# Kernel optimization log

Hardware: AMD Instinct MI355X
Metric: run time of the kernel (lower is better)

## Reference

```python
import jax, jax.numpy as jnp
import numpy as np

B, N = 4, 2048
EMB, HID = 64, 256
LENGTHSCALES = (0.5, 1.0, 2.0, 4.0)
H = len(LENGTHSCALES)
HEAD = HID // H  # 64, divides evenly
LAYERS = 4
IN_DIM = 3 + EMB + 3
EPS_LN = 1e-5


def _layer_norm(x, g, b):
    mu = jnp.mean(x, axis=-1, keepdims=True)
    var = jnp.mean((x - mu) ** 2, axis=-1, keepdims=True)
    return (x - mu) * jax.lax.rsqrt(var + EPS_LN) * g + b


def setup_inputs() -> dict:
    key = jax.random.key(0)
    ks = iter(jax.random.split(key, 32))
    p = lambda shape, s=0.02: jax.random.normal(next(ks), shape, jnp.float32) * s
    inp = {
        "latent_vars": jax.random.normal(next(ks), (B, N, 3), jnp.float32),
        "x_coords": jax.random.normal(next(ks), (B, N, 3), jnp.float32),
        "atom_embeddings": jax.random.normal(next(ks), (B, N, EMB), jnp.float32),
        # input MLP
        "in_W": p((IN_DIM, HID)), "in_b": jnp.zeros((HID,), jnp.float32),
        # per-layer kernel attention: per-head value projections + output projection
        "val_W": p((LAYERS, H, HID, HEAD)), "val_b": jnp.zeros((LAYERS, H, HEAD), jnp.float32),
        "attn_W": p((LAYERS, H * HEAD, HID)), "attn_b": jnp.zeros((LAYERS, HID), jnp.float32),
        # layer norms
        "ln1_g": jnp.ones((LAYERS, HID), jnp.float32), "ln1_b": jnp.zeros((LAYERS, HID), jnp.float32),
        "ln2_g": jnp.ones((LAYERS, HID), jnp.float32), "ln2_b": jnp.zeros((LAYERS, HID), jnp.float32),
        # FFN (hidden -> 2*hidden -> hidden)
        "ffn_W1": p((LAYERS, HID, 2 * HID)), "ffn_b1": jnp.zeros((LAYERS, 2 * HID), jnp.float32),
        "ffn_W2": p((LAYERS, 2 * HID, HID)), "ffn_b2": jnp.zeros((LAYERS, HID), jnp.float32),
        # output MLP
        "out_W1": p((HID, HID)), "out_b1": jnp.zeros((HID,), jnp.float32),
        "out_W2": p((HID, 3)), "out_b2": jnp.zeros((3,), jnp.float32),
    }
    return inp


def _forward(latent_vars, x_coords, atom_embeddings, in_W, in_b, val_W, val_b,
             attn_W, attn_b, ln1_g, ln1_b, ln2_g, ln2_b,
             ffn_W1, ffn_b1, ffn_W2, ffn_b2, out_W1, out_b1, out_W2, out_b2):
    # input MLP
    x = jnp.concatenate([x_coords, atom_embeddings, latent_vars], axis=-1)  # [B,N,70]
    feats = jax.nn.relu(x @ in_W + in_b)  # [B,N,HID]

    # RBF attention weights depend only on coords + fixed lengthscales -> compute once
    diff = x_coords[:, :, None, :] - x_coords[:, None, :, :]  # [B,N,N,3]
    d2 = jnp.sum(diff * diff, axis=-1)  # [B,N,N]
    ls2 = jnp.asarray(LENGTHSCALES, jnp.float32) ** 2  # [H]
    A = jnp.exp(-d2[None, :, :, :] / ls2[:, None, None, None])  # [H,B,N,N]
    A = A / (jnp.sum(A, axis=-1, keepdims=True) + 1e-8)

    for l in range(LAYERS):
        V = jnp.einsum('bnf,hfd->bnhd', feats, val_W[l]) + val_b[l]  # [B,N,H,HEAD]
        att = jnp.einsum('hbij,bjhd->bihd', A, V)  # [B,N,H,HEAD]
        att = att.reshape(att.shape[0], att.shape[1], H * HEAD) @ attn_W[l] + attn_b[l]
        feats = _layer_norm(feats + att, ln1_g[l], ln1_b[l])
        h = jax.nn.relu(feats @ ffn_W1[l] + ffn_b1[l]) @ ffn_W2[l] + ffn_b2[l]
        feats = _layer_norm(feats + h, ln2_g[l], ln2_b[l])

    return jax.nn.relu(feats @ out_W1 + out_b1) @ out_W2 + out_b2  # [B,N,3]


def reference(latent_vars, x_coords, atom_embeddings, in_W, in_b, val_W, val_b,
              attn_W, attn_b, ln1_g, ln1_b, ln2_g, ln2_b,
              ffn_W1, ffn_b1, ffn_W2, ffn_b2, out_W1, out_b1, out_W2, out_b2):
    return _forward(latent_vars, x_coords, atom_embeddings, in_W, in_b, val_W, val_b,
                    attn_W, attn_b, ln1_g, ln1_b, ln2_g, ln2_b,
                    ffn_W1, ffn_b1, ffn_W2, ffn_b2, out_W1, out_b1, out_W2, out_b2)
```

## Files before the change

### kernel.cpp

```cpp
#include <hip/hip_runtime.h>

#define B_ 4
#define N_ 2048
#define R_ (B_ * N_)
#define HID_ 256
#define EMB_ 64
#define IN_DIM_ 70
#define H_ 4
#define HEAD_ 64
#define FFN_ 512
#define LAYERS_ 4

typedef __attribute__((ext_vector_type(8))) short short8;
typedef __attribute__((ext_vector_type(4))) float f32x4;
typedef unsigned short ushort;

static __device__ __forceinline__ ushort f2bf(float f) {
    unsigned u = __builtin_bit_cast(unsigned, f);
    u += 0x7fffu + ((u >> 16) & 1u);
    return (ushort)(u >> 16);
}
static __device__ __forceinline__ float bf2f(ushort u) {
    unsigned x = ((unsigned)u) << 16;
    return __builtin_bit_cast(float, x);
}

#define GLOAD_LDS16(g, l)                                              \
    __builtin_amdgcn_global_load_lds(                                  \
        (const __attribute__((address_space(1))) void*)(g),            \
        (__attribute__((address_space(3))) void*)(l), 16, 0, 0)

#define MFMA16(a, b, c) __builtin_amdgcn_mfma_f32_16x16x32_bf16(a, b, c, 0, 0, 0)

__global__ __launch_bounds__(256) void pack_weights(const float* __restrict__ valW,
                                                    const float* __restrict__ attnW,
                                                    const float* __restrict__ ffnW1,
                                                    const float* __restrict__ ffnW2,
                                                    const float* __restrict__ outW1,
                                                    ushort* __restrict__ wp) {
    int idx = blockIdx.x * 256 + threadIdx.x;
    float v;
    if (idx < 262144) {
        int l = idx >> 16, c = (idx >> 8) & 255, k = idx & 255;
        v = valW[((l * 4 + (c >> 6)) * 256 + k) * 64 + (c & 63)];
    } else if (idx < 524288) {
        int i2 = idx - 262144;
        int l = i2 >> 16, c = (i2 >> 8) & 255, k = i2 & 255;
        v = attnW[l * 65536 + k * 256 + c];
    } else if (idx < 1048576) {
        int i2 = idx - 524288;
        int l = i2 >> 17, c = (i2 >> 8) & 511, k = i2 & 255;
        v = ffnW1[l * 131072 + k * 512 + c];
    } else if (idx < 1572864) {
        int i2 = idx - 1048576;
        int l = i2 >> 17, c = (i2 >> 9) & 255, k = i2 & 511;
        v = ffnW2[l * 131072 + k * 256 + c];
    } else {
        int i2 = idx - 1572864;
        int c = i2 >> 8, k = i2 & 255;
        v = outW1[k * 256 + c];
    }
    wp[idx] = f2bf(v);
}

__global__ __launch_bounds__(256) void input_mlp(const float* __restrict__ xc,
                                                 const float* __restrict__ emb,
                                                 const float* __restrict__ lat,
                                                 const float* __restrict__ W,
                                                 const float* __restrict__ b,
                                                 float* __restrict__ feats,
                                                 ushort* __restrict__ featsb) {
    __shared__ float xr[8][IN_DIM_ + 2];
    int t = threadIdx.x;
    int row0 = blockIdx.x * 8;
    for (int idx = t; idx < 8 * IN_DIM_; idx += 256) {
        int r = idx / IN_DIM_, f = idx % IN_DIM_;
        int rr = row0 + r;
        float v;
        if (f < 3)       v = xc[rr * 3 + f];
        else if (f < 67) v = emb[rr * EMB_ + (f - 3)];
        else             v = lat[rr * 3 + (f - 67)];
        xr[r][f] = v;
    }
    __syncthreads();
    float acc[8] = {0.f, 0.f, 0.f, 0.f, 0.f, 0.f, 0.f, 0.f};
    for (int f = 0; f < IN_DIM_; ++f) {
        float w = W[f * HID_ + t];
#pragma unroll
        for (int r = 0; r < 8; ++r) acc[r] += xr[r][f] * w;
    }
    float bb = b[t];
#pragma unroll
    for (int r = 0; r < 8; ++r) {
        float v = fmaxf(acc[r] + bb, 0.f);
        feats[(row0 + r) * HID_ + t] = v;
        featsb[(row0 + r) * HID_ + t] = f2bf(v);
    }
}

__global__ __launch_bounds__(256) void ebuild(const float* __restrict__ xc,
                                              ushort* __restrict__ E) {
    __shared__ float4 civ[64];
    __shared__ float4 cjv[512];
    int t = threadIdx.x;
    int jb = blockIdx.x;
    int ibl = blockIdx.y;
    int b = blockIdx.z;
    const float* xb = xc + (size_t)b * N_ * 3;
    if (t < 64) {
        const float* p = &xb[(ibl * 64 + t) * 3];
        float x = p[0], y = p[1], z = p[2];
        civ[t] = make_float4(x, y, z, x * x + y * y + z * z);
    }
#pragma unroll
    for (int s = 0; s < 2; ++s) {
        int j = s * 256 + t;
        const float* p = &xb[(jb * 512 + j) * 3];
        float x = p[0], y = p[1], z = p[2];
        cjv[j] = make_float4(x, y, z, x * x + y * y + z * z);
    }
    __syncthreads();
    int lane = t & 63, ig = t >> 6;
    float4 cj[8];
#pragma unroll
    for (int e = 0; e < 8; ++e) cj[e] = cjv[lane * 8 + e];
    const float ch0 = -4.f * 1.44269504088896f;
    ushort* Ebase = E + ((size_t)b * 2048 + ibl * 64) * 2048 + (size_t)jb * 512 + lane * 8;

    for (int r = 0; r < 16; ++r) {
        int i = ig * 16 + r;
        float4 ci = civ[i];
        float d[8];
#pragma unroll
        for (int e = 0; e < 8; ++e)
            d[e] = (ci.w + cj[e].w) -
                   2.f * (ci.x * cj[e].x + ci.y * cj[e].y + ci.z * cj[e].z);
        float ch = ch0;
#pragma unroll
        for (int h = 0; h < 4; ++h) {
            float ex[8];
#pragma unroll
            for (int e = 0; e < 8; ++e) ex[e] = exp2f(d[e] * ch);
            union { unsigned u[4]; uint4 v; } pk;
#pragma unroll
            for (int q = 0; q < 4; ++q)
                asm("v_cvt_pk_bf16_f32 %0, %1, %2"
                    : "=v"(pk.u[q]) : "v"(ex[2 * q]), "v"(ex[2 * q + 1]));
            *(uint4*)(Ebase + (size_t)h * 4 * 2048 * 2048 + (size_t)i * 2048) = pk.v;
            ch *= 0.25f;
        }
    }
}

__global__ __launch_bounds__(256, 2) void pv_gemm(const ushort* __restrict__ E,
                                                  const ushort* __restrict__ Vt,
                                                  ushort* __restrict__ attb) {
    __shared__ __align__(16) char lds[65536];
    int t = threadIdx.x;
    int l = t & 63, w = t >> 6;
    int lr = l & 15, g = l >> 4;

    int f = blockIdx.x;
    int xcd = f & 7, s = f >> 3;
    int combo = xcd * 2 + (s >> 5);
    int ib = s & 31;
    int b = combo & 3, h = combo >> 2;
    int i_base = ib * 64;
    int hc = h * 64;

    const ushort* Eb = E + (size_t)(h * 4 + b) * 2048 * 2048;
    int slot = t & 7, trow = t >> 3;

    const ushort* srcA[2];
    const ushort* srcB[2];
#pragma unroll
    for (int q = 0; q < 2; ++q) {
        int arw = q * 32 + trow;
        srcA[q] = Eb + (size_t)(i_base + arw) * 2048 + ((slot ^ (arw & 7)) << 3);
        srcB[q] = Vt + (size_t)(b * 256 + hc + arw) * 2048 + ((slot ^ (arw & 7)) << 3);
    }
    auto STAGE = [&](int c) {
        int buf = c & 3;
#pragma unroll
        for (int q = 0; q < 2; ++q)
            GLOAD_LDS16(srcA[q] + c * 64, lds + buf * 16384 + q * 4096 + t * 16);
#pragma unroll
        for (int q = 0; q < 2; ++q)
            GLOAD_LDS16(srcB[q] + c * 64, lds + buf * 16384 + 8192 + q * 4096 + t * 16);
    };

    f32x4 acc[4] = {};
    f32x4 accd = {};
    short8 ones = {0x3F80, 0x3F80, 0x3F80, 0x3F80, 0x3F80, 0x3F80, 0x3F80, 0x3F80};

    int arow = w * 16 + lr;
    int aoff = arow * 128;
    int sw_a = (arow & 7) << 4;

    auto COMPUTE = [&](int c) {
        const char* As = lds + (c & 3) * 16384;
        const char* Bs = As + 8192;
        short8 a0 = *(const short8*)(As + aoff + ((g * 16) ^ sw_a));
        short8 a1 = *(const short8*)(As + aoff + ((64 + g * 16) ^ sw_a));
        accd = MFMA16(a0, ones, accd);
        accd = MFMA16(a1, ones, accd);
#pragma unroll
        for (int n = 0; n < 4; ++n) {
            int cc = n * 16 + lr;
            const char* cb = Bs + cc * 128;
            int sw = (cc & 7) << 4;
            short8 b0 = *(const short8*)(cb + ((g * 16) ^ sw));
            short8 b1 = *(const short8*)(cb + ((64 + g * 16) ^ sw));
            acc[n] = MFMA16(a0, b0, acc[n]);
            acc[n] = MFMA16(a1, b1, acc[n]);
        }
    };

    STAGE(0);
    STAGE(1);
    STAGE(2);

    for (int c = 0; c < 30; ++c) {
        asm volatile("s_waitcnt vmcnt(8)" ::: "memory");
        __builtin_amdgcn_s_barrier();
        __builtin_amdgcn_sched_barrier(0);
        if (c < 29) STAGE(c + 3);
        COMPUTE(c);
    }
    asm volatile("s_waitcnt vmcnt(4)" ::: "memory");
    __builtin_amdgcn_s_barrier();
    __builtin_amdgcn_sched_barrier(0);
    COMPUTE(30);
    asm volatile("s_waitcnt vmcnt(0)" ::: "memory");
    __builtin_amdgcn_s_barrier();
    __builtin_amdgcn_sched_barrier(0);
    COMPUTE(31);

#pragma unroll
    for (int r = 0; r < 4; ++r) {
        float invd = 1.f / (accd[r] + 1e-8f);
        int row = i_base + w * 16 + g * 4 + r;
        size_t rb = ((size_t)b * N_ + row) * 256 + hc + lr;
#pragma unroll
        for (int n = 0; n < 4; ++n)
            attb[rb + n * 16] = f2bf(acc[n][r] * invd);
    }
}

template <int MODE>
__global__ __launch_bounds__(256) void gemmM(const ushort* __restrict__ A,
                                             const ushort* __restrict__ Bt,
                                             const float* __restrict__ bias,
                                             const float* __restrict__ resid,
                                             const float* __restrict__ lng,
                                             ushort* __restrict__ outb,
                                             float* __restrict__ outf) {
    __shared__ __align__(16) char lds[69632];
    int t = threadIdx.x;
    int l = t & 63, w = t >> 6;
    int lr = l & 15, g = l >> 4;
    int row0 = blockIdx.x * 16;
    f32x4 acc[4] = {};

    const ushort* srcA = A + (size_t)(row0 + (t >> 3)) * 256 + (((t & 7) ^ ((t >> 3) & 7)) << 3);
    const ushort* srcB[8];
#pragma unroll
    for (int q = 0; q < 8; ++q) {
        int cl = q * 32 + (t >> 3);
        srcB[q] = Bt + (size_t)cl * 256 + (((t & 7) ^ (cl & 7)) << 3);
    }
    auto STAGE = [&](int buf) {
        if (t < 128) GLOAD_LDS16(srcA, lds + buf * 2048 + t * 16);
#pragma unroll
        for (int q = 0; q < 8; ++q)
            GLOAD_LDS16(srcB[q], lds + 4096 + buf * 32768 + q * 4096 + t * 16);
        srcA += 64;
#pragma unroll
        for (int q = 0; q < 8; ++q) srcB[q] += 64;
    };

    int sw_a = (lr & 7) << 4;
    int aoff = lr * 128;

    STAGE(0);
#pragma unroll
    for (int c = 0; c < 4; ++c) {
        __syncthreads();
        if (c + 1 < 4) STAGE((c + 1) & 1);
        const char* As = lds + (c & 1) * 2048;
        const char* Ws = lds + 4096 + (c & 1) * 32768;

        short8 a0 = *(const short8*)(As + aoff + ((g * 16) ^ sw_a));
        short8 a1 = *(const short8*)(As + aoff + ((64 + g * 16) ^ sw_a));
#pragma unroll
        for (int n = 0; n < 4; ++n) {
            int cc = w * 64 + n * 16 + lr;
            const char* cb = Ws + cc * 128;
            int sw = (cc & 7) << 4;
            short8 b0 = *(const short8*)(cb + ((g * 16) ^ sw));
            short8 b1 = *(const short8*)(cb + ((64 + g * 16) ^ sw));
            acc[n] = MFMA16(a0, b0, acc[n]);
            acc[n] = MFMA16(a1, b1, acc[n]);
        }
    }
    __syncthreads();

    if constexpr (MODE == 3) {
        ushort(*Ts)[24] = (ushort(*)[24])lds;
#pragma unroll
        for (int n = 0; n < 4; ++n) {
            int c = w * 64 + n * 16 + lr;
            float bi = bias[c];
#pragma unroll
            for (int r = 0; r < 4; ++r)
                Ts[c][g * 4 + r] = f2bf(acc[n][r] + bi);
        }
        __syncthreads();
        {
            int c = t;
            int b = row0 >> 11;
            int n0 = row0 & 2047;
            ushort* dst = outb + ((size_t)(b * 256 + c)) * 2048 + n0;
            *(uint4*)dst = *(uint4*)&Ts[c][0];
            *(uint4*)(dst + 8) = *(uint4*)&Ts[c][8];
        }
    } else {
        const float* W2 = resid;
        const float* b2 = lng;
        ushort(*Ts)[264] = (ushort(*)[264])lds;
#pragma unroll
        for (int n = 0; n < 4; ++n) {
            int c = w * 64 + n * 16 + lr;
            float bi = bias[c];
#pragma unroll
            for (int r = 0; r < 4; ++r)
                Ts[g * 4 + r][c] = f2bf(fmaxf(acc[n][r] + bi, 0.f));
        }
        __syncthreads();
        int row = t >> 4, sg = t & 15;
        float p0 = 0.f, p1 = 0.f, p2 = 0.f;
#pragma unroll
        for (int e = 0; e < 16; ++e) {
            float x = bf2f(Ts[row][sg * 16 + e]);
            const float* wr = &W2[(sg * 16 + e) * 3];
            p0 += x * wr[0];
            p1 += x * wr[1];
            p2 += x * wr[2];
        }
#pragma unroll
        for (int off = 1; off < 16; off <<= 1) {
            p0 += __shfl_xor(p0, off, 64);
            p1 += __shfl_xor(p1, off, 64);
            p2 += __shfl_xor(p2, off, 64);
        }
        if (sg == 0) {
            int gr = row0 + row;
            outf[gr * 3 + 0] = p0 + b2[0];
            outf[gr * 3 + 1] = p1 + b2[1];
            outf[gr * 3 + 2] = p2 + b2[2];
        }
    }
}

__global__ __launch_bounds__(512) void gemm_layer(
        const ushort* __restrict__ attb,
        const ushort* __restrict__ Wat, const float* __restrict__ pb,
        float* __restrict__ feats,
        const float* __restrict__ ln1g, const float* __restrict__ ln1b,
        const ushort* __restrict__ W1t, const float* __restrict__ b1,
        const ushort* __restrict__ W2t, const float* __restrict__ b2,
        const float* __restrict__ ln2g, const float* __restrict__ ln2b,
        ushort* __restrict__ featsb,
        const ushort* __restrict__ WvN, const float* __restrict__ vbN,
        ushort* __restrict__ Vt) {
    __shared__ __align__(16) char lds[122880];
    char* Aa = lds;
    char* Asp = lds + 8192;
    char* Wsp = lds + 24576;
    char* hidp = lds + 90112;

    int t = threadIdx.x;
    int l = t & 63, w = t >> 6;
    int cg = w & 3, mh = w >> 2;
    int lr = l & 15, g = l >> 4;
    int row0 = blockIdx.x * 32;
    int arow = mh * 16 + lr;
    int sw_a = (lr & 7) << 4;
    int trow = t >> 3, slot = t & 7;

    uint4 wA0, wA1, wA2, wA3;
    uint4 wB0, wB1, wB2, wB3;
    auto WLOADA = [&](const ushort* Wb, int stride, int colbase, int c) {
        const ushort* base = Wb + c * 64;
#pragma unroll
        for (int q = 0; q < 4; ++q) {
            int cl = colbase + q * 64 + trow;
            uint4 v = *(const uint4*)(base + (size_t)cl * stride + ((slot ^ (cl & 7)) << 3));
            if (q == 0) wA0 = v; else if (q == 1) wA1 = v;
            else if (q == 2) wA2 = v; else wA3 = v;
        }
    };
    auto WLOADB = [&](const ushort* Wb, int stride, int colbase, int c) {
        const ushort* base = Wb + c * 64;
#pragma unroll
        for (int q = 0; q < 4; ++q) {
            int cl = colbase + q * 64 + trow;
            uint4 v = *(const uint4*)(base + (size_t)cl * stride + ((slot ^ (cl & 7)) << 3));
            if (q == 0) wB0 = v; else if (q == 1) wB1 = v;
            else if (q == 2) wB2 = v; else wB3 = v;
        }
    };
    auto WSTOREA = [&]() {
        *(uint4*)(Wsp + 0 * 8192 + t * 16) = wA0;
        *(uint4*)(Wsp + 1 * 8192 + t * 16) = wA1;
        *(uint4*)(Wsp + 2 * 8192 + t * 16) = wA2;
        *(uint4*)(Wsp + 3 * 8192 + t * 16) = wA3;
    };
    auto WSTOREB = [&]() {
        char* base = Wsp + 32768;
        *(uint4*)(base + 0 * 8192 + t * 16) = wB0;
        *(uint4*)(base + 1 * 8192 + t * 16) = wB1;
        *(uint4*)(base + 2 * 8192 + t * 16) = wB2;
        *(uint4*)(base + 3 * 8192 + t * 16) = wB3;
    };

    const ushort* srcA = attb + (size_t)(row0 + trow) * 256 + ((slot ^ (trow & 7)) << 3);
    auto STAGEA = [&](int buf, int c) {
        if (t < 256) GLOAD_LDS16(srcA + c * 64, Aa + buf * 4096 + t * 16);
    };

    f32x4 acc0[4] = {};
    STAGEA(0, 0);
    WLOADA(Wat, 256, 0, 0);
#pragma unroll
    for (int c = 0; c < 4; ++c) {
        __syncthreads();
        WSTOREA();
        __syncthreads();
        if (c < 3) { WLOADA(Wat, 256, 0, c + 1); STAGEA((c + 1) & 1, c + 1); }
        else WLOADA(W1t, 256, 0, 0);

        const char* As = Aa + (c & 1) * 4096;
        short8 a0 = *(const short8*)(As + arow * 128 + ((g * 16) ^ sw_a));
        short8 a1 = *(const short8*)(As + arow * 128 + ((64 + g * 16) ^ sw_a));
#pragma unroll
        for (int n = 0; n < 4; ++n) {
            int cc = cg * 64 + n * 16 + lr;
            const char* cb = Wsp + cc * 128;
            int sw = (cc & 7) << 4;
            short8 b0 = *(const short8*)(cb + ((g * 16) ^ sw));
            short8 b1 = *(const short8*)(cb + ((64 + g * 16) ^ sw));
            acc0[n] = MFMA16(a0, b0, acc0[n]);
            acc0[n] = MFMA16(a1, b1, acc0[n]);
        }
    }
    __syncthreads();

    float* red1 = (float*)lds;
    float* red2 = (float*)(lds + 512);
    float x1v[4][4];
    {
        float s1[4] = {0.f, 0.f, 0.f, 0.f}, s2[4] = {0.f, 0.f, 0.f, 0.f};
#pragma unroll
        for (int n = 0; n < 4; ++n) {
            int c = cg * 64 + n * 16 + lr;
            float bi = pb[c];
#pragma unroll
            for (int r = 0; r < 4; ++r) {
                int row = row0 + mh * 16 + g * 4 + r;
                float v = acc0[n][r] + bi + feats[(size_t)row * 256 + c];
                x1v[n][r] = v;
                s1[r] += v;
                s2[r] += v * v;
            }
        }
#pragma unroll
        for (int off = 1; off < 16; off <<= 1) {
#pragma unroll
            for (int r = 0; r < 4; ++r) {
                s1[r] += __shfl_xor(s1[r], off, 64);
                s2[r] += __shfl_xor(s2[r], off, 64);
            }
        }
        if (lr == 0) {
#pragma unroll
            for (int r = 0; r < 4; ++r) {
                red1[(mh * 16 + g * 4 + r) * 4 + cg] = s1[r];
                red2[(mh * 16 + g * 4 + r) * 4 + cg] = s2[r];
            }
        }
        __syncthreads();
#pragma unroll
        for (int n = 0; n < 4; ++n) {
            int c = cg * 64 + n * 16 + lr;
            float gg = ln1g[c], bb = ln1b[c];
#pragma unroll
            for (int r = 0; r < 4; ++r) {
                int rr = mh * 16 + g * 4 + r;
                float m1 = red1[rr * 4] + red1[rr * 4 + 1] + red1[rr * 4 + 2] + red1[rr * 4 + 3];
                float m2 = red2[rr * 4] + red2[rr * 4 + 1] + red2[rr * 4 + 2] + red2[rr * 4 + 3];
                float mu = m1 * (1.f / 256.f);
                float var = m2 * (1.f / 256.f) - mu * mu;
                float rstd = rsqrtf(var + 1e-5f);
                float o = (x1v[n][r] - mu) * rstd * gg + bb;
                x1v[n][r] = o;
                *(ushort*)(Asp + rr * 512 + ((2 * c) ^ ((rr & 7) << 4))) = f2bf(o);
            }
        }
    }

    WSTOREA();
    WLOADB(W1t, 256, 0, 1);
    asm volatile("s_waitcnt lgkmcnt(0)" ::: "memory");
    __builtin_amdgcn_sched_barrier(0);
    __builtin_amdgcn_s_barrier();

    f32x4 acc1[4] = {}, acc1b[4] = {}, acc2[4] = {};
#pragma unroll
    for (int u = 0; u < 16; ++u) {
        const char* WB = Wsp + (u & 1) * 32768;
        short8 a0, a1;
        if (u < 8) {
            int c = u & 3;
            a0 = *(const short8*)(Asp + arow * 512 + ((c * 128 + g * 16) ^ sw_a));
            a1 = *(const short8*)(Asp + arow * 512 + ((c * 128 + 64 + g * 16) ^ sw_a));
        } else {
            int c = u - 8;
            a0 = *(const short8*)(hidp + arow * 1024 + ((c * 128 + g * 16) ^ sw_a));
            a1 = *(const short8*)(hidp + arow * 1024 + ((c * 128 + 64 + g * 16) ^ sw_a));
        }
#pragma unroll
        for (int n = 0; n < 4; ++n) {
            int cc = cg * 64 + n * 16 + lr;
            const char* cb = WB + cc * 128;
            int sw = (cc & 7) << 4;
            short8 b0 = *(const short8*)(cb + ((g * 16) ^ sw));
            short8 b1 = *(const short8*)(cb + ((64 + g * 16) ^ sw));
            if (u < 4)      { acc1[n] = MFMA16(a0, b0, acc1[n]);  acc1[n] = MFMA16(a1, b1, acc1[n]); }
            else if (u < 8) { acc1b[n] = MFMA16(a0, b0, acc1b[n]); acc1b[n] = MFMA16(a1, b1, acc1b[n]); }
            else            { acc2[n] = MFMA16(a0, b0, acc2[n]);  acc2[n] = MFMA16(a1, b1, acc2[n]); }
        }
        if (u == 3) {
#pragma unroll
            for (int n = 0; n < 4; ++n) {
                int cf = cg * 64 + n * 16 + lr;
                float bi = b1[cf];
#pragma unroll
                for (int r = 0; r < 4; ++r) {
                    int rw = mh * 16 + g * 4 + r;
                    float v = fmaxf(acc1[n][r] + bi, 0.f);
                    *(ushort*)(hidp + rw * 1024 + ((cf * 2) ^ ((rw & 7) << 4))) = f2bf(v);
                }
            }
        }
        if (u == 7) {
#pragma unroll
            for (int n = 0; n < 4; ++n) {
                int cf = 256 + cg * 64 + n * 16 + lr;
                float bi = b1[cf];
#pragma unroll
                for (int r = 0; r < 4; ++r) {
                    int rw = mh * 16 + g * 4 + r;
                    float v = fmaxf(acc1b[n][r] + bi, 0.f);
                    *(ushort*)(hidp + rw * 1024 + ((cf * 2) ^ ((rw & 7) << 4))) = f2bf(v);
                }
            }
        }
        {
            int k = u + 2;
            bool issued = true;
            if (k < 4)       { if (u & 1) WLOADB(W1t, 256, 0, k);       else WLOADA(W1t, 256, 0, k); }
            else if (k < 8)  { if (u & 1) WLOADB(W1t, 256, 256, k - 4); else WLOADA(W1t, 256, 256, k - 4); }
            else if (k < 16) { if (u & 1) WLOADB(W2t, 512, 0, k - 8);   else WLOADA(W2t, 512, 0, k - 8); }
            else if (WvN)    { if (u & 1) WLOADB(WvN, 256, 0, k - 16);  else WLOADA(WvN, 256, 0, k - 16); }
            else issued = false;
            if (issued) asm volatile("s_waitcnt vmcnt(4)" ::: "memory");
            else        asm volatile("s_waitcnt vmcnt(0)" ::: "memory");
            __builtin_amdgcn_sched_barrier(0);
            if (u < 15 || WvN) { if ((u + 1) & 1) WSTOREB(); else WSTOREA(); }
            asm volatile("s_waitcnt lgkmcnt(0)" ::: "memory");
            __builtin_amdgcn_sched_barrier(0);
            __builtin_amdgcn_s_barrier();
        }
    }

#pragma unroll
    for (int n = 0; n < 4; ++n) {
        int c = cg * 64 + n * 16 + lr;
        float bi = b2[c];
#pragma unroll
        for (int r = 0; r < 4; ++r)
            acc2[n][r] = acc2[n][r] + bi + x1v[n][r];
    }
    {
        float* red1b = (float*)lds;
        float* red2b = (float*)(lds + 512);
        float s1[4] = {0.f, 0.f, 0.f, 0.f}, s2[4] = {0.f, 0.f, 0.f, 0.f};
#pragma unroll
        for (int n = 0; n < 4; ++n)
#pragma unroll
            for (int r = 0; r < 4; ++r) {
                s1[r] += acc2[n][r];
                s2[r] += acc2[n][r] * acc2[n][r];
            }
#pragma unroll
        for (int off = 1; off < 16; off <<= 1) {
#pragma unroll
            for (int r = 0; r < 4; ++r) {
                s1[r] += __shfl_xor(s1[r], off, 64);
                s2[r] += __shfl_xor(s2[r], off, 64);
            }
        }
        if (lr == 0) {
#pragma unroll
            for (int r = 0; r < 4; ++r) {
                red1b[(mh * 16 + g * 4 + r) * 4 + cg] = s1[r];
                red2b[(mh * 16 + g * 4 + r) * 4 + cg] = s2[r];
            }
        }
        __syncthreads();
#pragma unroll
        for (int n = 0; n < 4; ++n) {
            int c = cg * 64 + n * 16 + lr;
            float gg = ln2g[c], bb = ln2b[c];
#pragma unroll
            for (int r = 0; r < 4; ++r) {
                int rr = mh * 16 + g * 4 + r;
                float m1 = red1b[rr * 4] + red1b[rr * 4 + 1] + red1b[rr * 4 + 2] + red1b[rr * 4 + 3];
                float m2 = red2b[rr * 4] + red2b[rr * 4 + 1] + red2b[rr * 4 + 2] + red2b[rr * 4 + 3];
                float mu = m1 * (1.f / 256.f);
                float var = m2 * (1.f / 256.f) - mu * mu;
                float rstd = rsqrtf(var + 1e-5f);
                int row = row0 + rr;
                float o = (acc2[n][r] - mu) * rstd * gg + bb;
                feats[(size_t)row * 256 + c] = o;
                ushort ob = f2bf(o);
                featsb[(size_t)row * 256 + c] = ob;
                *(ushort*)(Asp + rr * 512 + ((2 * c) ^ ((rr & 7) << 4))) = ob;
            }
        }
    }
    __syncthreads();

    if (WvN) {
        f32x4 acc3[4] = {};
#pragma unroll
        for (int u3 = 0; u3 < 4; ++u3) {
            const char* WB = Wsp + (u3 & 1) * 32768;
            short8 a0 = *(const short8*)(Asp + arow * 512 + ((u3 * 128 + g * 16) ^ sw_a));
            short8 a1 = *(const short8*)(Asp + arow * 512 + ((u3 * 128 + 64 + g * 16) ^ sw_a));
#pragma unroll
            for (int n = 0; n < 4; ++n) {
                int cc = cg * 64 + n * 16 + lr;
                const char* cb = WB + cc * 128;
                int sw = (cc & 7) << 4;
                short8 b0 = *(const short8*)(cb + ((g * 16) ^ sw));
                short8 b1 = *(const short8*)(cb + ((64 + g * 16) ^ sw));
                acc3[n] = MFMA16(a0, b0, acc3[n]);
                acc3[n] = MFMA16(a1, b1, acc3[n]);
            }
            if (u3 < 3) {
                if (u3 < 2) {
                    if (u3 & 1) WLOADB(WvN, 256, 0, u3 + 2);
                    else        WLOADA(WvN, 256, 0, u3 + 2);
                    asm volatile("s_waitcnt vmcnt(4)" ::: "memory");
                } else {
                    asm volatile("s_waitcnt vmcnt(0)" ::: "memory");
                }
                __builtin_amdgcn_sched_barrier(0);
                if ((u3 + 1) & 1) WSTOREB(); else WSTOREA();
                asm volatile("s_waitcnt lgkmcnt(0)" ::: "memory");
                __builtin_amdgcn_sched_barrier(0);
                __builtin_amdgcn_s_barrier();
            }
        }
        __syncthreads();
        ushort(*Ts)[40] = (ushort(*)[40])hidp;
#pragma unroll
        for (int n = 0; n < 4; ++n) {
            int c = cg * 64 + n * 16 + lr;
            float bi = vbN[c];
#pragma unroll
            for (int r = 0; r < 4; ++r)
                Ts[c][mh * 16 + g * 4 + r] = f2bf(acc3[n][r] + bi);
        }
        __syncthreads();
        if (t < 256) {
            int c = t;
            int b = row0 >> 11;
            int n0 = row0 & 2047;
            ushort* dst = Vt + ((size_t)(b * 256 + c)) * 2048 + n0;
            *(uint4*)dst = *(uint4*)&Ts[c][0];
            *(uint4*)(dst + 8) = *(uint4*)&Ts[c][8];
            *(uint4*)(dst + 16) = *(uint4*)&Ts[c][16];
            *(uint4*)(dst + 24) = *(uint4*)&Ts[c][24];
        }
    }
}

extern "C" void kernel_launch(void* const* d_in, const int* in_sizes, int n_in,
                              void* d_out, int out_size, void* d_ws, size_t ws_size,
                              hipStream_t stream) {
    const float* lat    = (const float*)d_in[0];
    const float* xc     = (const float*)d_in[1];
    const float* emb    = (const float*)d_in[2];
    const float* in_W   = (const float*)d_in[3];
    const float* in_b   = (const float*)d_in[4];
    const float* val_W  = (const float*)d_in[5];
    const float* val_b  = (const float*)d_in[6];
    const float* attn_W = (const float*)d_in[7];
    const float* attn_b = (const float*)d_in[8];
    const float* ln1_g  = (const float*)d_in[9];
    const float* ln1_b  = (const float*)d_in[10];
    const float* ln2_g  = (const float*)d_in[11];
    const float* ln2_b  = (const float*)d_in[12];
    const float* ffn_W1 = (const float*)d_in[13];
    const float* ffn_b1 = (const float*)d_in[14];
    const float* ffn_W2 = (const float*)d_in[15];
    const float* ffn_b2 = (const float*)d_in[16];
    const float* out_W1 = (const float*)d_in[17];
    const float* out_b1 = (const float*)d_in[18];
    const float* out_W2 = (const float*)d_in[19];
    const float* out_b2 = (const float*)d_in[20];

    char* W = (char*)d_ws;
    float*  feats  = (float*)W;
    ushort* featsb = (ushort*)(W + (8u << 20));
    ushort* attb   = (ushort*)(W + (12u << 20));
    ushort* Vt     = (ushort*)(W + (16u << 20));
    ushort* wp     = (ushort*)(W + (20u << 20));
    ushort* E      = (ushort*)(W + (24u << 20));
    ushort* Wvt  = wp;
    ushort* Wat  = wp + 262144;
    ushort* W1t  = wp + 524288;
    ushort* W2t  = wp + 1048576;
    ushort* Wo1t = wp + 1572864;

    pack_weights<<<6400, 256, 0, stream>>>(val_W, attn_W, ffn_W1, ffn_W2, out_W1, wp);
    input_mlp<<<R_ / 8, 256, 0, stream>>>(xc, emb, lat, in_W, in_b, feats, featsb);
    ebuild<<<dim3(4, 32, B_), 256, 0, stream>>>(xc, E);

    gemmM<3><<<R_ / 16, 256, 0, stream>>>(
        featsb, Wvt, val_b, nullptr, nullptr, Vt, nullptr);

    for (int l = 0; l < LAYERS_; ++l) {
        pv_gemm<<<512, 256, 0, stream>>>(E, Vt, attb);
        const ushort* WvN = (l + 1 < LAYERS_) ? (Wvt + (l + 1) * 65536) : nullptr;
        const float* vbN = val_b + ((l + 1 < LAYERS_) ? (l + 1) * 256 : 0);
        gemm_layer<<<R_ / 32, 512, 0, stream>>>(
            attb, Wat + l * 65536, attn_b + l * 256,
            feats, ln1_g + l * 256, ln1_b + l * 256,
            W1t + l * 131072, ffn_b1 + l * 512,
            W2t + l * 131072, ffn_b2 + l * 256,
            ln2_g + l * 256, ln2_b + l * 256,
            featsb, WvN, vbN, Vt);
    }

    gemmM<4><<<R_ / 16, 256, 0, stream>>>(
        featsb, Wo1t, out_b1, out_W2, out_b2, nullptr, (float*)d_out);
}
```

Before: 243.5 us.

## Double pv_gemm row tile to 128 rows per block for V reuse

```diff
diff --git a/kernel.cpp b/kernel.cpp
--- a/kernel.cpp
+++ b/kernel.cpp
@@ -152,58 +152,67 @@
     }
 }
 
-__global__ __launch_bounds__(256, 2) void pv_gemm(const ushort* __restrict__ E,
+__global__ __launch_bounds__(256, 1) void pv_gemm(const ushort* __restrict__ E,
                                                   const ushort* __restrict__ Vt,
                                                   ushort* __restrict__ attb) {
-    __shared__ __align__(16) char lds[65536];
+    __shared__ __align__(16) char lds[98304];
     int t = threadIdx.x;
     int l = t & 63, w = t >> 6;
     int lr = l & 15, g = l >> 4;
 
     int f = blockIdx.x;
     int xcd = f & 7, s = f >> 3;
-    int combo = xcd * 2 + (s >> 5);
-    int ib = s & 31;
+    int combo = xcd * 2 + (s >> 4);
+    int ib = s & 15;
     int b = combo & 3, h = combo >> 2;
-    int i_base = ib * 64;
+    int i_base = ib * 128;
     int hc = h * 64;
 
     const ushort* Eb = E + (size_t)(h * 4 + b) * 2048 * 2048;
-    int slot = t & 7, trow = t >> 3;
-
-    const ushort* srcA[2];
+
+    const ushort* srcA[4];
     const ushort* srcB[2];
 #pragma unroll
+    for (int q = 0; q < 4; ++q) {
+        int slotq = q * 256 + t;
+        int arw = slotq >> 3, sl = slotq & 7;
+        srcA[q] = Eb + (size_t)(i_base + arw) * 2048 + ((sl ^ (arw & 7)) << 3);
+    }
+#pragma unroll
     for (int q = 0; q < 2; ++q) {
-        int arw = q * 32 + trow;
-        srcA[q] = Eb + (size_t)(i_base + arw) * 2048 + ((slot ^ (arw & 7)) << 3);
-        srcB[q] = Vt + (size_t)(b * 256 + hc + arw) * 2048 + ((slot ^ (arw & 7)) << 3);
+        int slotq = q * 256 + t;
+        int crw = slotq >> 3, sl = slotq & 7;
+        srcB[q] = Vt + (size_t)(b * 256 + hc + crw) * 2048 + ((sl ^ (crw & 7)) << 3);
     }
     auto STAGE = [&](int c) {
-        int buf = c & 3;
+        char* base = lds + (c & 3) * 24576;
+#pragma unroll
+        for (int q = 0; q < 4; ++q)
+            GLOAD_LDS16(srcA[q] + c * 64, base + (q * 256 + t) * 16);
 #pragma unroll
         for (int q = 0; q < 2; ++q)
-            GLOAD_LDS16(srcA[q] + c * 64, lds + buf * 16384 + q * 4096 + t * 16);
-#pragma unroll
-        for (int q = 0; q < 2; ++q)
-            GLOAD_LDS16(srcB[q] + c * 64, lds + buf * 16384 + 8192 + q * 4096 + t * 16);
+            GLOAD_LDS16(srcB[q] + c * 64, base + 16384 + (q * 256 + t) * 16);
     };
 
-    f32x4 acc[4] = {};
-    f32x4 accd = {};
+    f32x4 acc[2][4] = {};
+    f32x4 accd[2] = {};
     short8 ones = {0x3F80, 0x3F80, 0x3F80, 0x3F80, 0x3F80, 0x3F80, 0x3F80, 0x3F80};
 
-    int arow = w * 16 + lr;
-    int aoff = arow * 128;
-    int sw_a = (arow & 7) << 4;
+    int sw_a = (lr & 7) << 4;
+    int aoff0 = (w * 32 + lr) * 128;
+    int aoff1 = (w * 32 + 16 + lr) * 128;
 
     auto COMPUTE = [&](int c) {
-        const char* As = lds + (c & 3) * 16384;
-        const char* Bs = As + 8192;
-        short8 a0 = *(const short8*)(As + aoff + ((g * 16) ^ sw_a));
-        short8 a1 = *(const short8*)(As + aoff + ((64 + g * 16) ^ sw_a));
-        accd = MFMA16(a0, ones, accd);
-        accd = MFMA16(a1, ones, accd);
+        const char* As = lds + (c & 3) * 24576;
+        const char* Bs = As + 16384;
+        short8 a00 = *(const short8*)(As + aoff0 + ((g * 16) ^ sw_a));
+        short8 a01 = *(const short8*)(As + aoff0 + ((64 + g * 16) ^ sw_a));
+        short8 a10 = *(const short8*)(As + aoff1 + ((g * 16) ^ sw_a));
+        short8 a11 = *(const short8*)(As + aoff1 + ((64 + g * 16) ^ sw_a));
+        accd[0] = MFMA16(a00, ones, accd[0]);
+        accd[0] = MFMA16(a01, ones, accd[0]);
+        accd[1] = MFMA16(a10, ones, accd[1]);
+        accd[1] = MFMA16(a11, ones, accd[1]);
 #pragma unroll
         for (int n = 0; n < 4; ++n) {
             int cc = n * 16 + lr;
@@ -211,8 +220,10 @@
             int sw = (cc & 7) << 4;
             short8 b0 = *(const short8*)(cb + ((g * 16) ^ sw));
             short8 b1 = *(const short8*)(cb + ((64 + g * 16) ^ sw));
-            acc[n] = MFMA16(a0, b0, acc[n]);
-            acc[n] = MFMA16(a1, b1, acc[n]);
+            acc[0][n] = MFMA16(a00, b0, acc[0][n]);
+            acc[0][n] = MFMA16(a01, b1, acc[0][n]);
+            acc[1][n] = MFMA16(a10, b0, acc[1][n]);
+            acc[1][n] = MFMA16(a11, b1, acc[1][n]);
         }
     };
 
@@ -221,13 +232,13 @@
     STAGE(2);
 
     for (int c = 0; c < 30; ++c) {
-        asm volatile("s_waitcnt vmcnt(8)" ::: "memory");
+        asm volatile("s_waitcnt vmcnt(12)" ::: "memory");
         __builtin_amdgcn_s_barrier();
         __builtin_amdgcn_sched_barrier(0);
         if (c < 29) STAGE(c + 3);
         COMPUTE(c);
     }
-    asm volatile("s_waitcnt vmcnt(4)" ::: "memory");
+    asm volatile("s_waitcnt vmcnt(6)" ::: "memory");
     __builtin_amdgcn_s_barrier();
     __builtin_amdgcn_sched_barrier(0);
     COMPUTE(30);
@@ -237,13 +248,16 @@
     COMPUTE(31);
 
 #pragma unroll
-    for (int r = 0; r < 4; ++r) {
-        float invd = 1.f / (accd[r] + 1e-8f);
-        int row = i_base + w * 16 + g * 4 + r;
-        size_t rb = ((size_t)b * N_ + row) * 256 + hc + lr;
-#pragma unroll
-        for (int n = 0; n < 4; ++n)
-            attb[rb + n * 16] = f2bf(acc[n][r] * invd);
+    for (int m = 0; m < 2; ++m) {
+#pragma unroll
+        for (int r = 0; r < 4; ++r) {
+            float invd = 1.f / (accd[m][r] + 1e-8f);
+            int row = i_base + w * 32 + m * 16 + g * 4 + r;
+            size_t rb = ((size_t)b * N_ + row) * 256 + hc + lr;
+#pragma unroll
+            for (int n = 0; n < 4; ++n)
+                attb[rb + n * 16] = f2bf(acc[m][n][r] * invd);
+        }
     }
 }
 
@@ -744,7 +758,7 @@
         featsb, Wvt, val_b, nullptr, nullptr, Vt, nullptr);
 
     for (int l = 0; l < LAYERS_; ++l) {
-        pv_gemm<<<512, 256, 0, stream>>>(E, Vt, attb);
+        pv_gemm<<<256, 256, 0, stream>>>(E, Vt, attb);
         const ushort* WvN = (l + 1 < LAYERS_) ? (Wvt + (l + 1) * 65536) : nullptr;
         const float* vbN = val_b + ((l + 1 < LAYERS_) ? (l + 1) * 256 : 0);
         gemm_layer<<<R_ / 32, 512, 0, stream>>>(
```

Result: no change. 244.9 us (+0.5%).
